# Kernel tuning notes

Hardware: AMD Instinct MI355X
Metric: run time of the kernel (lower is better)

The kernel has to match this reference:

```python
import jax, jax.numpy as jnp
import numpy as np

B, D_IN, L = 32, 64, 4096
H = 256      # d_model
N2 = 32      # d_state // 2 (complex conjugate pairs)
NL = 4       # n_layers
D_OUT = 2
LN_EPS = 1e-5


def setup_inputs() -> dict:
    key = jax.random.key(0)
    ks = jax.random.split(key, 12)
    dt_min, dt_max = 1e-3, 1e-1
    log_dt = jax.random.uniform(ks[0], (NL, H)) * (np.log(dt_max) - np.log(dt_min)) + np.log(dt_min)
    C = jax.random.normal(ks[1], (NL, H, N2, 2))            # view_as_real of complex C
    log_A_real = jnp.log(0.5 * jnp.ones((NL, H, N2)))
    A_imag = jnp.pi * jnp.broadcast_to(jnp.arange(N2, dtype=jnp.float32), (NL, H, N2))
    Dskip = jax.random.normal(ks[2], (NL, H))
    glu_w = jax.random.normal(ks[3], (NL, 2 * H, H)) * (1.0 / np.sqrt(H))  # Conv1d(h,2h,1)
    glu_b = jnp.zeros((NL, 2 * H))
    ln_g = jnp.ones((NL, H))
    ln_b = jnp.zeros((NL, H))
    enc_w = jax.random.normal(ks[4], (D_IN, H)) * (1.0 / np.sqrt(D_IN))
    enc_b = jnp.zeros((H,))
    dec_w = jax.random.normal(ks[5], (H, D_OUT)) * (1.0 / np.sqrt(H))
    dec_b = jnp.zeros((D_OUT,))
    x = jax.random.normal(ks[6], (B, D_IN, L), dtype=jnp.float32)
    return dict(x=x, enc_w=enc_w, enc_b=enc_b, log_dt=log_dt, C=C,
                log_A_real=log_A_real, A_imag=A_imag, Dskip=Dskip,
                glu_w=glu_w, glu_b=glu_b, ln_g=ln_g, ln_b=ln_b,
                dec_w=dec_w, dec_b=dec_b)


def _s4d_layer(u, log_dt, C, log_A_real, A_imag, Dskip, glu_w, glu_b):
    # u: (B, H, L)
    Lx = u.shape[-1]
    dt = jnp.exp(log_dt)                              # (H,)
    Cc = C[..., 0] + 1j * C[..., 1]                   # (H, N2) complex
    A = -jnp.exp(log_A_real) + 1j * A_imag            # (H, N2)
    dtA = A * dt[:, None]                             # (H, N2)
    # Vandermonde kernel: exp(dtA * l) for l in [0, L)
    K = jnp.exp(dtA[:, :, None] * jnp.arange(Lx))     # (H, N2, L) complex
    Ct = Cc * (jnp.exp(dtA) - 1.0) / A                # ZOH discretization of C
    k = 2.0 * jnp.einsum('hn,hnl->hl', Ct, K).real    # (H, L) real SSM kernel
    # FFT-based causal convolution (circular conv of zero-padded signals)
    n = 2 * Lx
    kf = jnp.fft.rfft(k, n=n)                         # (H, L+1)
    uf = jnp.fft.rfft(u, n=n)                         # (B, H, L+1)
    y = jnp.fft.irfft(uf * kf, n=n)[..., :Lx]         # (B, H, L)
    y = y + u * Dskip[:, None]                        # skip connection
    y = jax.nn.gelu(y, approximate=False)
    # Conv1d(h, 2h, kernel_size=1) + GLU(dim=-2)
    z = jnp.einsum('oh,bhl->bol', glu_w, y) + glu_b[:, None]
    a, g = jnp.split(z, 2, axis=1)
    return a * jax.nn.sigmoid(g)


def reference(x, enc_w, enc_b, log_dt, C, log_A_real, A_imag, Dskip,
              glu_w, glu_b, ln_g, ln_b, dec_w, dec_b):
    # encoder: transpose -> Linear -> transpose, fused as channel einsum
    h = jnp.einsum('bcl,cd->bdl', x, enc_w) + enc_b[:, None]   # (B, H, L)
    for i in range(NL):
        res = h
        y = _s4d_layer(h, log_dt[i], C[i], log_A_real[i], A_imag[i],
                       Dskip[i], glu_w[i], glu_b[i])
        h = y + res
        # post-norm LayerNorm over channel dim (dropout is identity at p-eval)
        mu = h.mean(axis=1, keepdims=True)
        var = jnp.mean((h - mu) ** 2, axis=1, keepdims=True)
        h = (h - mu) / jnp.sqrt(var + LN_EPS) * ln_g[i][:, None] + ln_b[i][:, None]
    pooled = h.mean(axis=-1)                                   # mean over time L -> (B, H)
    logits = pooled @ dec_w + dec_b                            # (B, D_OUT)
    return jax.nn.softmax(logits, axis=1)
```

## Files before the change

kernel.cpp:

```cpp
#include <hip/hip_runtime.h>
#include <math.h>

#define B_    32
#define DIN   64
#define LSEQ  4096
#define H_    256
#define N2_   32
#define NL_   4
#define DOUT  2
#define LN_EPSF 1e-5f

typedef __bf16 bf16x8 __attribute__((ext_vector_type(8)));
typedef float  f32x4  __attribute__((ext_vector_type(4)));

__device__ inline unsigned short f2bf(float f) {
  unsigned u = __builtin_bit_cast(unsigned, f);
  u += 0x7FFFu + ((u >> 16) & 1u);
  return (unsigned short)(u >> 16);
}
__device__ inline float bf2f(unsigned short u) {
  return __builtin_bit_cast(float, ((unsigned)u) << 16);
}

__device__ inline void mode_params(const float* log_dt, const float* Cri,
                                   const float* lAr, const float* Aim,
                                   int layer, int hh, int n, float dt,
                                   float& dr, float& di, float& ctr, float& cti) {
  int idx = (layer * H_ + hh) * N2_ + n;
  float Are = -expf(lAr[idx]);
  float Aimv = Aim[idx];
  dr = Are * dt; di = Aimv * dt;
  float er = expf(dr), sn, cs;
  sincosf(di, &sn, &cs);
  float arr = er * cs, aii = er * sn;
  float nr = arr - 1.f, ni = aii;
  float inv = 1.f / (Are * Are + Aimv * Aimv);
  float qr = (nr * Are + ni * Aimv) * inv;
  float qi = (ni * Are - nr * Aimv) * inv;
  float Cr = Cri[2 * idx], Ci = Cri[2 * idx + 1];
  ctr = 2.f * (Cr * qr - Ci * qi);
  cti = 2.f * (Cr * qi + Ci * qr);
}

__global__ __launch_bounds__(64) void k_prep(
    const float* __restrict__ log_dt, const float* __restrict__ Cri,
    const float* __restrict__ lAr, const float* __restrict__ Aim,
    unsigned short* __restrict__ TtG, unsigned short* __restrict__ WinG,
    unsigned short* __restrict__ WhiG, unsigned short* __restrict__ WloG,
    float2* __restrict__ AQG)
{
  int bid = blockIdx.x;
  int layer = bid >> 8, hh = bid & 255;
  int lane = threadIdx.x;
  __shared__ float Kf[64];
  float dt = expf(log_dt[layer * H_ + hh]);

  float kd = 0.f;
  for (int n = 0; n < N2_; ++n) {
    float dr, di, ctr, cti;
    mode_params(log_dt, Cri, lAr, Aim, layer, hh, n, dt, dr, di, ctr, cti);
    float er = expf(dr * (float)lane), sn, cs;
    sincosf(di * (float)lane, &sn, &cs);
    kd += ctr * (er * cs) - cti * (er * sn);
  }
  Kf[lane] = kd;
  if (lane < N2_) {
    int idx = (layer * H_ + hh) * N2_ + lane;
    float dr64 = -expf(lAr[idx]) * dt * 64.f;
    float di64 = Aim[idx] * dt * 64.f;
    float er = expf(dr64), sn, cs;
    sincosf(di64, &sn, &cs);
    AQG[bid * N2_ + lane] = make_float2(er * cs, er * sn);
  }
  __syncthreads();

  size_t base = (size_t)bid * 4096;
  for (int t = 0; t < 64; ++t) {
    float v = (t <= lane) ? Kf[lane - t] : 0.f;
    TtG[base + lane * 64 + (((t >> 3) ^ (lane & 7)) << 3) + (t & 7)] = f2bf(v);
  }
  {
    int n = lane >> 1, im = lane & 1;
    float dr, di, ctr, cti;
    mode_params(log_dt, Cri, lAr, Aim, layer, hh, n, dt, dr, di, ctr, cti);
    for (int t = 0; t < 64; ++t) {
      float e = (float)(63 - t);
      float er = expf(dr * e), sn, cs;
      sincosf(di * e, &sn, &cs);
      float v = im ? (er * sn) : (er * cs);
      WinG[base + lane * 64 + (((t >> 3) ^ (lane & 7)) << 3) + (t & 7)] = f2bf(v);
    }
  }
  for (int r = 0; r < 64; ++r) {
    int n = r >> 1;
    float dr, di, ctr, cti;
    mode_params(log_dt, Cri, lAr, Aim, layer, hh, n, dt, dr, di, ctr, cti);
    float e = (float)(lane + 1);
    float er = expf(dr * e), sn, cs;
    sincosf(di * e, &sn, &cs);
    float wre = ctr * (er * cs) - cti * (er * sn);
    float wim = ctr * (er * sn) + cti * (er * cs);
    float v = (r & 1) ? -wim : wre;
    unsigned short hi = f2bf(v);
    float lo = v - bf2f(hi);
    size_t off = base + lane * 64 + (((r >> 3) ^ (lane & 7)) << 3) + (r & 7);
    WhiG[off] = hi;
    WloG[off] = f2bf(lo);
  }
}

__global__ __launch_bounds__(256) void k_wconv(
    const float* __restrict__ gw, unsigned short* __restrict__ wb)
{
  int t = blockIdx.x * 256 + threadIdx.x;
  int uu = t & 7;
  int r  = (t >> 3) & 511;
  int l4 = t >> 12;
  int layer = l4 >> 2, kc4 = l4 & 3;
  int ksrc = kc4 * 64 + ((uu ^ (r & 7)) << 3);
  const float* src = gw + ((size_t)(layer * 512 + r)) * H_ + ksrc;
  unsigned short* dst = wb + (size_t)t * 8;
#pragma unroll
  for (int j = 0; j < 8; ++j) dst[j] = f2bf(src[j]);
}

__global__ __launch_bounds__(256) void k_encoder(
    const float* __restrict__ x, const float* __restrict__ ew,
    const float* __restrict__ eb, unsigned short* __restrict__ h)
{
  __shared__ __align__(16) float Wl[32][256];
  __shared__ __align__(16) float Xl[32][32];
  int tid = threadIdx.x;
  int blk = blockIdx.x;
  int b  = blk >> 7;
  int l0 = (blk & 127) << 5;
  int ty = tid >> 3;
  int tx = tid & 7;
  float acc[8][4];
#pragma unroll
  for (int i = 0; i < 8; ++i)
#pragma unroll
    for (int j = 0; j < 4; ++j) acc[i][j] = 0.f;

  for (int kc = 0; kc < DIN; kc += 32) {
    const float4* ew4 = (const float4*)(ew + kc * H_);
#pragma unroll
    for (int it = 0; it < 8; ++it) {
      int idx = tid + (it << 8);
      ((float4*)&Wl[0][0])[idx] = ew4[idx];
    }
    {
      int c = tid >> 3, p = (tid & 7) << 2;
      *(float4*)&Xl[c][p] =
          *(const float4*)(x + ((size_t)(b * DIN + kc + c)) * LSEQ + l0 + p);
    }
    __syncthreads();
#pragma unroll
    for (int k = 0; k < 32; ++k) {
      float4 w0 = *(float4*)&Wl[k][ty * 8];
      float4 w1 = *(float4*)&Wl[k][ty * 8 + 4];
      float4 xv = *(float4*)&Xl[k][tx * 4];
      float wvv[8] = {w0.x, w0.y, w0.z, w0.w, w1.x, w1.y, w1.z, w1.w};
      float xs[4]  = {xv.x, xv.y, xv.z, xv.w};
#pragma unroll
      for (int i = 0; i < 8; ++i)
#pragma unroll
        for (int j = 0; j < 4; ++j) acc[i][j] = fmaf(wvv[i], xs[j], acc[i][j]);
    }
    __syncthreads();
  }
#pragma unroll
  for (int i = 0; i < 8; ++i) {
    int d = ty * 8 + i;
    float bia = eb[d];
    ushort4 o;
    o.x = f2bf(acc[i][0] + bia); o.y = f2bf(acc[i][1] + bia);
    o.z = f2bf(acc[i][2] + bia); o.w = f2bf(acc[i][3] + bia);
    *(ushort4*)(h + ((size_t)(b * H_ + d)) * LSEQ + l0 + tx * 4) = o;
  }
}

__global__ __launch_bounds__(256, 4) void k_chunk(
    const unsigned short* __restrict__ hin, unsigned short* __restrict__ G,
    const unsigned short* __restrict__ TtG, const unsigned short* __restrict__ WinG,
    const unsigned short* __restrict__ WhiG, const unsigned short* __restrict__ WloG,
    const float2* __restrict__ AQG, const float* __restrict__ Dsk, int layer)
{
  __shared__ __align__(16) char smem[40960];
  char* Ul    = smem;
  char* TtL   = smem + 8192;
  char* WinL  = smem + 16384;
  float* BstT = (float*)(smem + 24576);
  char* ShiL  = smem + 24576;
  char* SloL  = smem + 32768;

  int tid = threadIdx.x;
  int w = tid >> 6, lane = tid & 63;
  int rg = lane >> 4, lc = lane & 15;
  int bid = blockIdx.x;
  int hh = bid >> 5, b = bid & 31;
  size_t wbase = ((size_t)(layer * H_ + hh)) * 4096;
  const unsigned short* Urow = hin + ((size_t)(b * H_ + hh)) * LSEQ;

#pragma unroll
  for (int it = 0; it < 2; ++it) {
    int idx = tid + (it << 8);
    int c = idx >> 3, uu = idx & 7;
    uint4 v = ((const uint4*)Urow)[idx];
    *(uint4*)(Ul + c * 128 + ((uu ^ (c & 7)) << 4)) = v;
    ((uint4*)TtL)[idx]  = ((const uint4*)(TtG + wbase))[idx];
    ((uint4*)WinL)[idx] = ((const uint4*)(WinG + wbase))[idx];
  }
  __syncthreads();

  f32x4 accY[4], accB[4];
#pragma unroll
  for (int nb = 0; nb < 4; ++nb) {
    accY[nb] = (f32x4){0.f, 0.f, 0.f, 0.f};
    accB[nb] = (f32x4){0.f, 0.f, 0.f, 0.f};
  }
#pragma unroll
  for (int ks = 0; ks < 2; ++ks) {
    int ca = w * 16 + lc;
    int u = ks * 4 + rg;
    bf16x8 A = *(const bf16x8*)(Ul + ca * 128 + ((u ^ (ca & 7)) << 4));
#pragma unroll
    for (int nb = 0; nb < 4; ++nb) {
      int col = nb * 16 + lc;
      bf16x8 Bt = *(const bf16x8*)(TtL + col * 128 + ((u ^ (col & 7)) << 4));
      bf16x8 Bw = *(const bf16x8*)(WinL + col * 128 + ((u ^ (col & 7)) << 4));
      accY[nb] = __builtin_amdgcn_mfma_f32_16x16x32_bf16(A, Bt, accY[nb], 0, 0, 0);
      accB[nb] = __builtin_amdgcn_mfma_f32_16x16x32_bf16(A, Bw, accB[nb], 0, 0, 0);
    }
  }
#pragma unroll
  for (int nb = 0; nb < 4; ++nb)
#pragma unroll
    for (int reg = 0; reg < 4; ++reg) {
      int r = nb * 16 + lc;
      int cc = w * 16 + rg * 4 + reg;
      BstT[r * 64 + (cc ^ ((r & 7) << 2))] = accB[nb][reg];
    }
  __syncthreads();

  float Sr[8], Si[8], Mr[8], Mi[8];
  int c = lane;
  {
    const float2* aqb = AQG + (size_t)(layer * H_ + hh) * N2_ + w * 8;
#pragma unroll
    for (int q = 0; q < 8; ++q) {
      float2 aq = aqb[q];
      Mr[q] = aq.x; Mi[q] = aq.y;
      int r0 = (w * 8 + q) * 2, r1 = r0 + 1;
      Sr[q] = BstT[r0 * 64 + (c ^ ((r0 & 7) << 2))];
      Si[q] = BstT[r1 * 64 + (c ^ ((r1 & 7) << 2))];
    }
  }
  uint4 wst[4];
#pragma unroll
  for (int i = 0; i < 2; ++i) {
    wst[i]     = ((const uint4*)(WhiG + wbase))[tid + (i << 8)];
    wst[i + 2] = ((const uint4*)(WloG + wbase))[tid + (i << 8)];
  }
  __syncthreads();

#pragma unroll
  for (int dd = 0; dd < 6; ++dd) {
    int d = 1 << dd;
#pragma unroll
    for (int q = 0; q < 8; ++q) {
      float pr = __shfl_up(Sr[q], (unsigned)d);
      float pi = __shfl_up(Si[q], (unsigned)d);
      if (lane >= d) {
        Sr[q] = fmaf(Mr[q], pr, fmaf(-Mi[q], pi, Sr[q]));
        Si[q] = fmaf(Mr[q], pi, fmaf(Mi[q], pr, Si[q]));
      }
      if (dd < 5) {
        float t = fmaf(Mr[q], Mr[q], -Mi[q] * Mi[q]);
        Mi[q] = 2.f * Mr[q] * Mi[q];
        Mr[q] = t;
      }
    }
  }
#pragma unroll
  for (int q = 0; q < 8; ++q) {
    float pr = __shfl_up(Sr[q], 1u);
    float pi = __shfl_up(Si[q], 1u);
    Sr[q] = (lane == 0) ? 0.f : pr;
    Si[q] = (lane == 0) ? 0.f : pi;
  }
#pragma unroll
  for (int q = 0; q < 8; ++q) {
    int n = w * 8 + q;
    unsigned short hr = f2bf(Sr[q]), hi_ = f2bf(Si[q]);
    unsigned hiw = (unsigned)hr | ((unsigned)hi_ << 16);
    unsigned low = (unsigned)f2bf(Sr[q] - bf2f(hr)) |
                   ((unsigned)f2bf(Si[q] - bf2f(hi_)) << 16);
    int boff = c * 128 + (((n >> 2) ^ (c & 7)) << 4) + (((2 * n) & 7) << 1);
    *(unsigned*)(ShiL + boff) = hiw;
    *(unsigned*)(SloL + boff) = low;
  }
#pragma unroll
  for (int i = 0; i < 2; ++i) {
    ((uint4*)TtL)[tid + (i << 8)]  = wst[i];
    ((uint4*)WinL)[tid + (i << 8)] = wst[i + 2];
  }
  __syncthreads();

#pragma unroll
  for (int ks = 0; ks < 2; ++ks) {
    int ca = w * 16 + lc;
    int u = ks * 4 + rg;
    bf16x8 Ah = *(const bf16x8*)(ShiL + ca * 128 + ((u ^ (ca & 7)) << 4));
    bf16x8 Al = *(const bf16x8*)(SloL + ca * 128 + ((u ^ (ca & 7)) << 4));
#pragma unroll
    for (int nb = 0; nb < 4; ++nb) {
      int col = nb * 16 + lc;
      bf16x8 Wh = *(const bf16x8*)(TtL + col * 128 + ((u ^ (col & 7)) << 4));
      bf16x8 Wl2 = *(const bf16x8*)(WinL + col * 128 + ((u ^ (col & 7)) << 4));
      accY[nb] = __builtin_amdgcn_mfma_f32_16x16x32_bf16(Ah, Wh, accY[nb], 0, 0, 0);
      accY[nb] = __builtin_amdgcn_mfma_f32_16x16x32_bf16(Al, Wh, accY[nb], 0, 0, 0);
      accY[nb] = __builtin_amdgcn_mfma_f32_16x16x32_bf16(Ah, Wl2, accY[nb], 0, 0, 0);
    }
  }
  __syncthreads();

  float dsk = Dsk[layer * H_ + hh];
  unsigned short* Yl = (unsigned short*)(smem + 24576);
#pragma unroll
  for (int nb = 0; nb < 4; ++nb) {
#pragma unroll
    for (int reg = 0; reg < 4; ++reg) {
      int cc = w * 16 + rg * 4 + reg;
      int i = nb * 16 + lc;
      unsigned short ub = *(unsigned short*)(
          Ul + cc * 128 + (((i >> 3) ^ (cc & 7)) << 4) + (i & 7) * 2);
      float yv = fmaf(dsk, bf2f(ub), accY[nb][reg]);
      float ge = 0.5f * yv * (1.f + erff(yv * 0.70710678118f));
      Yl[cc * 64 + i] = f2bf(ge);
    }
  }
  __syncthreads();
  unsigned short* Gr = G + ((size_t)(b * H_ + hh)) * LSEQ;
#pragma unroll
  for (int it = 0; it < 2; ++it) {
    int idx = tid + (it << 8);
    *(uint4*)(Gr + idx * 8) = ((uint4*)Yl)[idx];
  }
}

__global__ __launch_bounds__(512, 4) void k_glu(
    const unsigned short* __restrict__ Wb, const unsigned short* __restrict__ G,
    unsigned short* __restrict__ h, const float* __restrict__ gb,
    const float* __restrict__ lng, const float* __restrict__ lnb, int layer)
{
  extern __shared__ char smem[];
  char* WlB = smem;
  char* GlB = smem + 65536;
  float2* Red = (float2*)(smem + 65536 + 8192);

  int tid = threadIdx.x;
  int w = tid >> 6, lane = tid & 63;
  int b  = blockIdx.x >> 6;
  int l0 = (blockIdx.x & 63) << 6;
  int rgrp = lane >> 4, lc = lane & 15;

  f32x4 acc[4][4];
#pragma unroll
  for (int m = 0; m < 4; ++m)
#pragma unroll
    for (int n = 0; n < 4; ++n) acc[m][n] = (f32x4){0.f, 0.f, 0.f, 0.f};

  const unsigned short* wsrc = Wb + (size_t)(layer * 4) * 512 * 64;

  for (int kc4 = 0; kc4 < 4; ++kc4) {
    if (kc4) __syncthreads();
    const unsigned short* wc = wsrc + (size_t)kc4 * 512 * 64;
#pragma unroll
    for (int i = 0; i < 8; ++i) {
      int off = w * 8192 + i * 1024 + lane * 16;
      uint4 v = *(const uint4*)((const char*)wc + off);
      *(uint4*)(WlB + off) = v;
    }
    {
      int col = lane;
      int kc = kc4 * 64;
      size_t base = (size_t)(b * H_ + kc + w * 8) * LSEQ + l0 + col;
      unsigned v0 = G[base];
      unsigned v1 = G[base + (size_t)1 * LSEQ];
      unsigned v2 = G[base + (size_t)2 * LSEQ];
      unsigned v3 = G[base + (size_t)3 * LSEQ];
      unsigned v4 = G[base + (size_t)4 * LSEQ];
      unsigned v5 = G[base + (size_t)5 * LSEQ];
      unsigned v6 = G[base + (size_t)6 * LSEQ];
      unsigned v7 = G[base + (size_t)7 * LSEQ];
      unsigned pk0 = v0 | (v1 << 16), pk1 = v2 | (v3 << 16);
      unsigned pk2 = v4 | (v5 << 16), pk3 = v6 | (v7 << 16);
      *(uint4*)(GlB + col * 128 + ((w ^ (col & 7)) << 4)) =
          make_uint4(pk0, pk1, pk2, pk3);
    }
    __syncthreads();
#pragma unroll
    for (int ks = 0; ks < 2; ++ks) {
      int u = ks * 4 + rgrp;
      bf16x8 af[4], bff[4];
#pragma unroll
      for (int m = 0; m < 4; ++m) {
        int grow = ((m < 2) ? (w * 32 + m * 16) : (256 + w * 32 + (m - 2) * 16)) + lc;
        af[m] = *(const bf16x8*)(WlB + grow * 128 + ((u ^ (grow & 7)) << 4));
      }
#pragma unroll
      for (int n = 0; n < 4; ++n) {
        int gcol = n * 16 + lc;
        bff[n] = *(const bf16x8*)(GlB + gcol * 128 + ((u ^ (gcol & 7)) << 4));
      }
#pragma unroll
      for (int m = 0; m < 4; ++m)
#pragma unroll
        for (int n = 0; n < 4; ++n)
          acc[m][n] = __builtin_amdgcn_mfma_f32_16x16x32_bf16(
              af[m], bff[n], acc[m][n], 0, 0, 0);
    }
  }

  const float* gbL = gb + layer * 2 * H_;
  float out[2][4][4];
  float s[4], ss[4];
#pragma unroll
  for (int n = 0; n < 4; ++n) { s[n] = 0.f; ss[n] = 0.f; }
#pragma unroll
  for (int mA = 0; mA < 2; ++mA) {
#pragma unroll
    for (int reg = 0; reg < 4; ++reg) {
      int ch = w * 32 + mA * 16 + rgrp * 4 + reg;
      float ba = gbL[ch], bg = gbL[ch + H_];
#pragma unroll
      for (int n = 0; n < 4; ++n) {
        int col = n * 16 + lc;
        size_t off = (size_t)(b * H_ + ch) * LSEQ + l0 + col;
        float a = acc[mA][n][reg] + ba;
        float gv = acc[mA + 2][n][reg] + bg;
        float sg = 1.f / (1.f + expf(-gv));
        float o = fmaf(a, sg, bf2f(h[off]));
        out[mA][n][reg] = o;
        s[n] += o; ss[n] = fmaf(o, o, ss[n]);
      }
    }
  }
#pragma unroll
  for (int n = 0; n < 4; ++n) {
    s[n]  += __shfl_xor(s[n], 16);  s[n]  += __shfl_xor(s[n], 32);
    ss[n] += __shfl_xor(ss[n], 16); ss[n] += __shfl_xor(ss[n], 32);
  }
  if (lane < 16) {
#pragma unroll
    for (int n = 0; n < 4; ++n)
      Red[w * 64 + n * 16 + lane] = make_float2(s[n], ss[n]);
  }
  __syncthreads();
  float mu[4], rs[4];
#pragma unroll
  for (int n = 0; n < 4; ++n) {
    int col = n * 16 + lc;
    float ts = 0.f, tss = 0.f;
#pragma unroll
    for (int ww = 0; ww < 8; ++ww) {
      float2 v = Red[ww * 64 + col];
      ts += v.x; tss += v.y;
    }
    mu[n] = ts * (1.f / H_);
    rs[n] = rsqrtf(tss * (1.f / H_) - mu[n] * mu[n] + LN_EPSF);
  }
#pragma unroll
  for (int mA = 0; mA < 2; ++mA) {
#pragma unroll
    for (int reg = 0; reg < 4; ++reg) {
      int ch = w * 32 + mA * 16 + rgrp * 4 + reg;
      float lg = lng[layer * H_ + ch], lb = lnb[layer * H_ + ch];
#pragma unroll
      for (int n = 0; n < 4; ++n) {
        int col = n * 16 + lc;
        size_t off = (size_t)(b * H_ + ch) * LSEQ + l0 + col;
        h[off] = f2bf((out[mA][n][reg] - mu[n]) * rs[n] * lg + lb);
      }
    }
  }
}

__global__ __launch_bounds__(256) void k_pool(
    const unsigned short* __restrict__ h, float* __restrict__ P)
{
  int row = blockIdx.x * 4 + (threadIdx.x >> 6);
  int lane = threadIdx.x & 63;
  const uint4* src = (const uint4*)(h + (size_t)row * LSEQ);
  float s = 0.f;
#pragma unroll
  for (int i = 0; i < 8; ++i) {
    uint4 v = src[lane + i * 64];
    unsigned ws[4] = {v.x, v.y, v.z, v.w};
#pragma unroll
    for (int j = 0; j < 4; ++j) {
      s += bf2f((unsigned short)(ws[j] & 0xFFFFu));
      s += bf2f((unsigned short)(ws[j] >> 16));
    }
  }
#pragma unroll
  for (int d = 1; d < 64; d <<= 1) s += __shfl_xor(s, d);
  if (lane == 0) P[row] = s * (1.f / LSEQ);
}

__global__ __launch_bounds__(64) void k_dec(
    const float* __restrict__ P, const float* __restrict__ dw,
    const float* __restrict__ db, float* __restrict__ out)
{
  int b = blockIdx.x, lane = threadIdx.x;
  float z0 = 0.f, z1 = 0.f;
#pragma unroll
  for (int i = 0; i < 4; ++i) {
    int k = lane + i * 64;
    float p = P[b * H_ + k];
    z0 = fmaf(p, dw[k * DOUT + 0], z0);
    z1 = fmaf(p, dw[k * DOUT + 1], z1);
  }
#pragma unroll
  for (int d = 1; d < 64; d <<= 1) {
    z0 += __shfl_xor(z0, d);
    z1 += __shfl_xor(z1, d);
  }
  if (lane == 0) {
    z0 += db[0]; z1 += db[1];
    float m = fmaxf(z0, z1);
    float e0 = expf(z0 - m), e1 = expf(z1 - m);
    float inv = 1.f / (e0 + e1);
    out[b * 2 + 0] = e0 * inv;
    out[b * 2 + 1] = e1 * inv;
  }
}

extern "C" void kernel_launch(void* const* d_in, const int* in_sizes, int n_in,
                              void* d_out, int out_size, void* d_ws, size_t ws_size,
                              hipStream_t stream) {
  (void)in_sizes; (void)n_in; (void)out_size; (void)ws_size;
  const float* x      = (const float*)d_in[0];
  const float* enc_w  = (const float*)d_in[1];
  const float* enc_b  = (const float*)d_in[2];
  const float* log_dt = (const float*)d_in[3];
  const float* Cri    = (const float*)d_in[4];
  const float* lAr    = (const float*)d_in[5];
  const float* Aim    = (const float*)d_in[6];
  const float* Dsk    = (const float*)d_in[7];
  const float* glu_w  = (const float*)d_in[8];
  const float* glu_b  = (const float*)d_in[9];
  const float* ln_g   = (const float*)d_in[10];
  const float* ln_b   = (const float*)d_in[11];
  const float* dec_w  = (const float*)d_in[12];
  const float* dec_b  = (const float*)d_in[13];
  float* out = (float*)d_out;

  unsigned short* h   = (unsigned short*)d_ws;
  unsigned short* G   = h + (size_t)B_ * H_ * LSEQ;
  unsigned short* Wb  = G + (size_t)B_ * H_ * LSEQ;
  unsigned short* TtG = Wb + 524288;
  unsigned short* WinG = TtG + 4194304;
  unsigned short* WhiG = WinG + 4194304;
  unsigned short* WloG = WhiG + 4194304;
  float2* AQG = (float2*)(WloG + 4194304);
  float* P    = (float*)(AQG + NL_ * H_ * N2_);

  k_wconv<<<256, 256, 0, stream>>>(glu_w, Wb);
  k_prep<<<NL_ * H_, 64, 0, stream>>>(log_dt, Cri, lAr, Aim, TtG, WinG, WhiG, WloG, AQG);
  k_encoder<<<B_ * (LSEQ / 32), 256, 0, stream>>>(x, enc_w, enc_b, h);
  for (int i = 0; i < NL_; ++i) {
    k_chunk<<<H_ * B_, 256, 0, stream>>>(h, G, TtG, WinG, WhiG, WloG,
                                         AQG, Dsk, i);
    k_glu<<<B_ * (LSEQ / 64), 512, 77824, stream>>>(Wb, G, h, glu_b, ln_g, ln_b, i);
  }
  k_pool<<<(B_ * H_) / 4, 256, 0, stream>>>(h, P);
  k_dec<<<B_, 64, 0, stream>>>(P, dec_w, dec_b, out);
}
```

Measured before the change: 945.0 us.

## Store h pre-swizzled, use direct global-to-LDS loads, fold Dskip into kernel

Stores activations h in global memory already in the XOR-swizzled chunk layout, so k_chunk can copy rows straight into LDS with global_load_lds instead of staging them through registers. The Whi/Wlo and GLU weight loads are moved to the async global-to-LDS path as well. The D skip term is folded into the diagonal of the Toeplitz matrix, so the per-element skip FMA and extra LDS read go away. The exact erf and sigmoid are replaced by a polynomial erf approximation and fast exp/rcp, which adds approximation error in the GELU and GLU.

```diff
diff --git a/kernel.cpp b/kernel.cpp
--- a/kernel.cpp
+++ b/kernel.cpp
@@ -20,6 +20,24 @@
 }
 __device__ inline float bf2f(unsigned short u) {
   return __builtin_bit_cast(float, ((unsigned)u) << 16);
+}
+
+__device__ inline void gl_lds16(const void* g, void* l) {
+  __builtin_amdgcn_global_load_lds(
+      (const __attribute__((address_space(1))) void*)g,
+      (__attribute__((address_space(3))) void*)l, 16, 0, 0);
+}
+
+__device__ inline float erf_fast(float x) {
+  float ax = fabsf(x);
+  float t = __builtin_amdgcn_rcpf(fmaf(0.3275911f, ax, 1.f));
+  float p = fmaf(1.061405429f, t, -1.453152027f);
+  p = fmaf(p, t, 1.421413741f);
+  p = fmaf(p, t, -0.284496736f);
+  p = fmaf(p, t, 0.254829592f);
+  float e = __expf(-ax * ax);
+  float r = 1.f - p * t * e;
+  return copysignf(r, x);
 }
 
 __device__ inline void mode_params(const float* log_dt, const float* Cri,
@@ -45,6 +63,7 @@
 __global__ __launch_bounds__(64) void k_prep(
     const float* __restrict__ log_dt, const float* __restrict__ Cri,
     const float* __restrict__ lAr, const float* __restrict__ Aim,
+    const float* __restrict__ Dsk,
     unsigned short* __restrict__ TtG, unsigned short* __restrict__ WinG,
     unsigned short* __restrict__ WhiG, unsigned short* __restrict__ WloG,
     float2* __restrict__ AQG)
@@ -54,6 +73,7 @@
   int lane = threadIdx.x;
   __shared__ float Kf[64];
   float dt = expf(log_dt[layer * H_ + hh]);
+  float dsk = Dsk[layer * H_ + hh];
 
   float kd = 0.f;
   for (int n = 0; n < N2_; ++n) {
@@ -76,7 +96,7 @@
 
   size_t base = (size_t)bid * 4096;
   for (int t = 0; t < 64; ++t) {
-    float v = (t <= lane) ? Kf[lane - t] : 0.f;
+    float v = (t <= lane) ? (Kf[lane - t] + ((t == lane) ? dsk : 0.f)) : 0.f;
     TtG[base + lane * 64 + (((t >> 3) ^ (lane & 7)) << 3) + (t & 7)] = f2bf(v);
   }
   {
@@ -169,6 +189,11 @@
     }
     __syncthreads();
   }
+  int l = l0 + tx * 4;
+  int cch = l >> 6;
+  int uu  = (l & 63) >> 3;
+  int j8  = l & 7;
+  size_t soff = (cch << 6) + (((uu ^ (cch & 7))) << 3) + j8;
 #pragma unroll
   for (int i = 0; i < 8; ++i) {
     int d = ty * 8 + i;
@@ -176,7 +201,7 @@
     ushort4 o;
     o.x = f2bf(acc[i][0] + bia); o.y = f2bf(acc[i][1] + bia);
     o.z = f2bf(acc[i][2] + bia); o.w = f2bf(acc[i][3] + bia);
-    *(ushort4*)(h + ((size_t)(b * H_ + d)) * LSEQ + l0 + tx * 4) = o;
+    *(ushort4*)(h + ((size_t)(b * H_ + d)) * LSEQ + soff) = o;
   }
 }
 
@@ -184,7 +209,7 @@
     const unsigned short* __restrict__ hin, unsigned short* __restrict__ G,
     const unsigned short* __restrict__ TtG, const unsigned short* __restrict__ WinG,
     const unsigned short* __restrict__ WhiG, const unsigned short* __restrict__ WloG,
-    const float2* __restrict__ AQG, const float* __restrict__ Dsk, int layer)
+    const float2* __restrict__ AQG, int layer)
 {
   __shared__ __align__(16) char smem[40960];
   char* Ul    = smem;
@@ -205,11 +230,10 @@
 #pragma unroll
   for (int it = 0; it < 2; ++it) {
     int idx = tid + (it << 8);
-    int c = idx >> 3, uu = idx & 7;
-    uint4 v = ((const uint4*)Urow)[idx];
-    *(uint4*)(Ul + c * 128 + ((uu ^ (c & 7)) << 4)) = v;
-    ((uint4*)TtL)[idx]  = ((const uint4*)(TtG + wbase))[idx];
-    ((uint4*)WinL)[idx] = ((const uint4*)(WinG + wbase))[idx];
+    int ubase = (w * 64 + (it << 8)) * 16;
+    gl_lds16(((const uint4*)Urow) + idx, Ul + ubase);
+    gl_lds16(((const uint4*)(TtG + wbase)) + idx, TtL + ubase);
+    gl_lds16(((const uint4*)(WinG + wbase)) + idx, WinL + ubase);
   }
   __syncthreads();
 
@@ -243,6 +267,14 @@
     }
   __syncthreads();
 
+#pragma unroll
+  for (int it = 0; it < 2; ++it) {
+    int idx = tid + (it << 8);
+    int ubase = (w * 64 + (it << 8)) * 16;
+    gl_lds16(((const uint4*)(WhiG + wbase)) + idx, TtL + ubase);
+    gl_lds16(((const uint4*)(WloG + wbase)) + idx, WinL + ubase);
+  }
+
   float Sr[8], Si[8], Mr[8], Mi[8];
   int c = lane;
   {
@@ -255,12 +287,6 @@
       Sr[q] = BstT[r0 * 64 + (c ^ ((r0 & 7) << 2))];
       Si[q] = BstT[r1 * 64 + (c ^ ((r1 & 7) << 2))];
     }
-  }
-  uint4 wst[4];
-#pragma unroll
-  for (int i = 0; i < 2; ++i) {
-    wst[i]     = ((const uint4*)(WhiG + wbase))[tid + (i << 8)];
-    wst[i + 2] = ((const uint4*)(WloG + wbase))[tid + (i << 8)];
   }
   __syncthreads();
 
@@ -300,11 +326,6 @@
     *(unsigned*)(ShiL + boff) = hiw;
     *(unsigned*)(SloL + boff) = low;
   }
-#pragma unroll
-  for (int i = 0; i < 2; ++i) {
-    ((uint4*)TtL)[tid + (i << 8)]  = wst[i];
-    ((uint4*)WinL)[tid + (i << 8)] = wst[i + 2];
-  }
   __syncthreads();
 
 #pragma unroll
@@ -325,7 +346,6 @@
   }
   __syncthreads();
 
-  float dsk = Dsk[layer * H_ + hh];
   unsigned short* Yl = (unsigned short*)(smem + 24576);
 #pragma unroll
   for (int nb = 0; nb < 4; ++nb) {
@@ -333,10 +353,8 @@
     for (int reg = 0; reg < 4; ++reg) {
       int cc = w * 16 + rg * 4 + reg;
       int i = nb * 16 + lc;
-      unsigned short ub = *(unsigned short*)(
-          Ul + cc * 128 + (((i >> 3) ^ (cc & 7)) << 4) + (i & 7) * 2);
-      float yv = fmaf(dsk, bf2f(ub), accY[nb][reg]);
-      float ge = 0.5f * yv * (1.f + erff(yv * 0.70710678118f));
+      float yv = accY[nb][reg];
+      float ge = 0.5f * yv * (1.f + erf_fast(yv * 0.70710678118f));
       Yl[cc * 64 + i] = f2bf(ge);
     }
   }
@@ -364,6 +382,7 @@
   int b  = blockIdx.x >> 6;
   int l0 = (blockIdx.x & 63) << 6;
   int rgrp = lane >> 4, lc = lane & 15;
+  int cch = l0 >> 6, cs7 = cch & 7;
 
   f32x4 acc[4][4];
 #pragma unroll
@@ -378,9 +397,8 @@
     const unsigned short* wc = wsrc + (size_t)kc4 * 512 * 64;
 #pragma unroll
     for (int i = 0; i < 8; ++i) {
-      int off = w * 8192 + i * 1024 + lane * 16;
-      uint4 v = *(const uint4*)((const char*)wc + off);
-      *(uint4*)(WlB + off) = v;
+      int base = w * 8192 + i * 1024;
+      gl_lds16((const char*)wc + base + lane * 16, WlB + base);
     }
     {
       int col = lane;
@@ -423,6 +441,13 @@
     }
   }
 
+  int colS[4];
+#pragma unroll
+  for (int n = 0; n < 4; ++n) {
+    int col = n * 16 + lc;
+    colS[n] = ((((col >> 3) ^ cs7)) << 3) | (col & 7);
+  }
+
   const float* gbL = gb + layer * 2 * H_;
   float out[2][4][4];
   float s[4], ss[4];
@@ -436,11 +461,10 @@
       float ba = gbL[ch], bg = gbL[ch + H_];
 #pragma unroll
       for (int n = 0; n < 4; ++n) {
-        int col = n * 16 + lc;
-        size_t off = (size_t)(b * H_ + ch) * LSEQ + l0 + col;
+        size_t off = (size_t)(b * H_ + ch) * LSEQ + l0 + colS[n];
         float a = acc[mA][n][reg] + ba;
         float gv = acc[mA + 2][n][reg] + bg;
-        float sg = 1.f / (1.f + expf(-gv));
+        float sg = __builtin_amdgcn_rcpf(1.f + __expf(-gv));
         float o = fmaf(a, sg, bf2f(h[off]));
         out[mA][n][reg] = o;
         s[n] += o; ss[n] = fmaf(o, o, ss[n]);
@@ -479,8 +503,7 @@
       float lg = lng[layer * H_ + ch], lb = lnb[layer * H_ + ch];
 #pragma unroll
       for (int n = 0; n < 4; ++n) {
-        int col = n * 16 + lc;
-        size_t off = (size_t)(b * H_ + ch) * LSEQ + l0 + col;
+        size_t off = (size_t)(b * H_ + ch) * LSEQ + l0 + colS[n];
         h[off] = f2bf((out[mA][n][reg] - mu[n]) * rs[n] * lg + lb);
       }
     }
@@ -568,11 +591,11 @@
   float* P    = (float*)(AQG + NL_ * H_ * N2_);
 
   k_wconv<<<256, 256, 0, stream>>>(glu_w, Wb);
-  k_prep<<<NL_ * H_, 64, 0, stream>>>(log_dt, Cri, lAr, Aim, TtG, WinG, WhiG, WloG, AQG);
+  k_prep<<<NL_ * H_, 64, 0, stream>>>(log_dt, Cri, lAr, Aim, Dsk,
+                                      TtG, WinG, WhiG, WloG, AQG);
   k_encoder<<<B_ * (LSEQ / 32), 256, 0, stream>>>(x, enc_w, enc_b, h);
   for (int i = 0; i < NL_; ++i) {
-    k_chunk<<<H_ * B_, 256, 0, stream>>>(h, G, TtG, WinG, WhiG, WloG,
-                                         AQG, Dsk, i);
+    k_chunk<<<H_ * B_, 256, 0, stream>>>(h, G, TtG, WinG, WhiG, WloG, AQG, i);
     k_glu<<<B_ * (LSEQ / 64), 512, 77824, stream>>>(Wb, G, h, glu_b, ln_g, ln_b, i);
   }
   k_pool<<<(B_ * H_) / 4, 256, 0, stream>>>(h, P);
```

Measured after the change: 868.3 us. 8.1% less time.
